# Performance work log

Measured on AMD Instinct MI355X. Metric: run time of the kernel, lower is better.

## Reference

```python
import jax, jax.numpy as jnp
import numpy as np

N_NODES = 50000
N_EDGES = 1600000
N_GRAPHS = 512
HEADS = 4
HEAD_DIM = 32
LAYERS = 3
NEG_SLOPE = 0.2


def setup_inputs() -> dict:
    key = jax.random.key(0)
    ks = jax.random.split(key, 7)
    x = jax.random.normal(ks[0], (N_NODES, 128), dtype=jnp.float32)
    Ws = jax.random.normal(ks[1], (LAYERS, 128, 128), dtype=jnp.float32) * 0.1
    att_src = jax.random.normal(ks[2], (LAYERS, HEADS, HEAD_DIM), dtype=jnp.float32) * 0.1
    att_dst = jax.random.normal(ks[3], (LAYERS, HEADS, HEAD_DIM), dtype=jnp.float32) * 0.1
    biases = jnp.zeros((LAYERS, 128), dtype=jnp.float32)
    edge_index = jax.random.randint(ks[4], (2, N_EDGES), 0, N_NODES, dtype=jnp.int64)
    batch = jnp.sort(jax.random.randint(ks[5], (N_NODES,), 0, N_GRAPHS, dtype=jnp.int64))
    return {"x": x, "Ws": Ws, "att_src": att_src, "att_dst": att_dst,
            "biases": biases, "edge_index": edge_index, "batch": batch}


def _gat_layer(x, W, a_s, a_d, b, src, dst, n):
    # linear transform -> per-head features [N, H, C]
    h = (x @ W).reshape(n, HEADS, HEAD_DIM)
    # per-node attention halves [N, H]
    alpha_src = jnp.einsum('nhc,hc->nh', h, a_s)
    alpha_dst = jnp.einsum('nhc,hc->nh', h, a_d)
    # edge logits [E, H]
    e = jax.nn.leaky_relu(alpha_src[src] + alpha_dst[dst], NEG_SLOPE)
    # segment softmax over incoming edges of each destination node
    m = jax.ops.segment_max(e, dst, num_segments=n)
    w = jnp.exp(e - m[dst])
    denom = jax.ops.segment_sum(w, dst, num_segments=n)
    alpha = w / (denom[dst] + 1e-16)
    # weighted scatter-add of source features [E, H, C] -> [N, H, C]
    msg = h[src] * alpha[:, :, None]
    out = jax.ops.segment_sum(msg, dst, num_segments=n)
    return out.reshape(n, HEADS * HEAD_DIM) + b


def reference(x, Ws, att_src, att_dst, biases, edge_index, batch):
    n = x.shape[0]
    # PyG GATConv adds self-loops by default
    loops = jnp.arange(n, dtype=edge_index.dtype)
    src = jnp.concatenate([edge_index[0], loops])
    dst = jnp.concatenate([edge_index[1], loops])
    for l in range(LAYERS):
        x = jax.nn.elu(_gat_layer(x, Ws[l], att_src[l], att_dst[l], biases[l], src, dst, n))
        # dropout is identity in eval mode
    # global mean pool over graphs
    sums = jax.ops.segment_sum(x, batch, num_segments=N_GRAPHS)
    cnt = jax.ops.segment_sum(jnp.ones((n,), x.dtype), batch, num_segments=N_GRAPHS)
    return sums / jnp.maximum(cnt, 1.0)[:, None]
```

## Files before the change

### kernel.cpp

```cpp
#include <hip/hip_runtime.h>
#include <hip/hip_fp16.h>
#include <math.h>

#define HEADS 4
#define HDIM 32
#define FD 128
#define NEG 0.2f
#define BCAP 4608
#define CH 8192
#define CHW 128

typedef _Float16 f16x8 __attribute__((ext_vector_type(8)));
typedef float f32x4 __attribute__((ext_vector_type(4)));

__device__ __forceinline__ float lrelu(float x) { return fmaxf(x, NEG * x); }

__global__ __launch_bounds__(256) void k_prepW(const float* __restrict__ W,
                                               _Float16* __restrict__ W16T) {
    int l = blockIdx.x;
    const float* Wl = W + (long)l * FD * FD;
    _Float16* o = W16T + (long)l * FD * FD;
    for (int i = threadIdx.x; i < FD * FD; i += 256) {
        int k = i >> 7, n = i & 127;
        o[n * FD + k] = (_Float16)Wl[i];
    }
}

__global__ __launch_bounds__(256) void k_cvt(const float* __restrict__ x,
                                             __half* __restrict__ o, long n) {
    long i = ((long)blockIdx.x * 256 + threadIdx.x) * 4;
    if (i < n) {
        float4 v = *(const float4*)&x[i];
        *(__half2*)&o[i] = __floats2half2_rn(v.x, v.y);
        *(__half2*)&o[i + 2] = __floats2half2_rn(v.z, v.w);
    }
}

__global__ __launch_bounds__(256) void k_gemm_mfma(const __half* __restrict__ x16,
                                                   const _Float16* __restrict__ W16T,
                                                   __half* __restrict__ h, int N) {
    __shared__ _Float16 wl[FD * FD];
    int t = threadIdx.x;
    for (int i = t * 8; i < FD * FD; i += 2048)
        *(f16x8*)&wl[i] = *(const f16x8*)&W16T[i];

    int w = t >> 6, lane = t & 63;
    int m = lane & 15, quad = lane >> 4;
    int row0 = blockIdx.x * 128 + w * 32;

    f16x8 a[2][4];
    f16x8 zf = {};
#pragma unroll
    for (int rt = 0; rt < 2; ++rt) {
        int gr = row0 + rt * 16 + m;
#pragma unroll
        for (int kc = 0; kc < 4; ++kc)
            a[rt][kc] = (gr < N) ? *(const f16x8*)&x16[(long)gr * FD + kc * 32 + quad * 8] : zf;
    }
    f32x4 acc[2][8];
#pragma unroll
    for (int rt = 0; rt < 2; ++rt)
#pragma unroll
        for (int c = 0; c < 8; ++c) acc[rt][c] = (f32x4){0.f, 0.f, 0.f, 0.f};

    __syncthreads();
#pragma unroll
    for (int c = 0; c < 8; ++c) {
        int nb = c * 16 + m;
#pragma unroll
        for (int kc = 0; kc < 4; ++kc) {
            f16x8 b = *(f16x8*)&wl[nb * FD + kc * 32 + quad * 8];
            acc[0][c] = __builtin_amdgcn_mfma_f32_16x16x32_f16(a[0][kc], b, acc[0][c], 0, 0, 0);
            acc[1][c] = __builtin_amdgcn_mfma_f32_16x16x32_f16(a[1][kc], b, acc[1][c], 0, 0, 0);
        }
    }
#pragma unroll
    for (int rt = 0; rt < 2; ++rt) {
        int rbase = row0 + rt * 16 + quad * 4;
#pragma unroll
        for (int c = 0; c < 8; ++c) {
            int col = c * 16 + m;
#pragma unroll
            for (int i = 0; i < 4; ++i) {
                int gr = rbase + i;
                if (gr < N) h[(long)gr * FD + col] = __float2half(acc[rt][c][i]);
            }
        }
    }
}

__global__ __launch_bounds__(256) void k_alpha(const __half* __restrict__ h,
                                               const float* __restrict__ a_s,
                                               const float* __restrict__ a_d,
                                               float* __restrict__ as_o,
                                               float* __restrict__ ad_o, int N) {
    int t = threadIdx.x;
    int n = blockIdx.x * 16 + (t >> 4);
    if (n >= N) return;
    int c16 = t & 15, gh = c16 >> 2, cb = c16 * 8;
    int c32 = (c16 & 3) * 8;
    float4 raw = *(const float4*)&h[(long)n * FD + cb];
    const __half* hh = (const __half*)&raw;
    float vs = 0.f, vd = 0.f;
#pragma unroll
    for (int i = 0; i < 8; ++i) {
        float hv = __half2float(hh[i]);
        vs += hv * a_s[gh * HDIM + c32 + i];
        vd += hv * a_d[gh * HDIM + c32 + i];
    }
    vs += __shfl_xor(vs, 1); vs += __shfl_xor(vs, 2);
    vd += __shfl_xor(vd, 1); vd += __shfl_xor(vd, 2);
    if ((c16 & 3) == 0) {
        as_o[n * HEADS + gh] = vs;
        ad_o[n * HEADS + gh] = vd;
    }
}

__global__ void k_zero_f(float* __restrict__ p, long n) {
    long i = (long)blockIdx.x * 256 + threadIdx.x;
    if (i < n) p[i] = 0.f;
}
__global__ void k_zero_i(int* __restrict__ p, int n) {
    int i = blockIdx.x * 256 + threadIdx.x;
    if (i < n) p[i] = 0;
}

__global__ __launch_bounds__(1024) void k_bin(const int* __restrict__ ei, int NE,
                                              int nbuck,
                                              int* __restrict__ bcnt,
                                              int* __restrict__ binned) {
    __shared__ int hist[512];
    __shared__ int gbase[512];
    int t = threadIdx.x;
    int c0 = blockIdx.x * CH;
    if (t < 512) hist[t] = 0;
    __syncthreads();
    int sub[8], val[8], loff[8];
#pragma unroll
    for (int k = 0; k < 8; ++k) {
        int idx = c0 + k * 1024 + t;
        sub[k] = -1;
        if (idx < NE) {
            int s = ei[idx], d = ei[NE + idx];
            sub[k] = d >> 7;
            val[k] = s | ((d & 127) << 16);
            loff[k] = atomicAdd(&hist[sub[k]], 1);
        }
    }
    __syncthreads();
    if (t < 512 && t < nbuck && hist[t] > 0)
        gbase[t] = atomicAdd(&bcnt[t], hist[t]);
    __syncthreads();
#pragma unroll
    for (int k = 0; k < 8; ++k) {
        if (sub[k] >= 0) {
            int p = gbase[sub[k]] + loff[k];
            if (p < BCAP) binned[(long)sub[k] * BCAP + p] = val[k];
        }
    }
}

__global__ __launch_bounds__(1024) void k_scan_sub(const int* __restrict__ bcnt,
                                                   int* __restrict__ bbase, int n,
                                                   int* __restrict__ rowstart, int N, int NE) {
    __shared__ int sm[1024];
    int t = threadIdx.x;
    int c0 = t * 4;
    int v0 = (c0 < n) ? bcnt[c0] : 0;
    int v1 = (c0 + 1 < n) ? bcnt[c0 + 1] : 0;
    int v2 = (c0 + 2 < n) ? bcnt[c0 + 2] : 0;
    int v3 = (c0 + 3 < n) ? bcnt[c0 + 3] : 0;
    int tot = v0 + v1 + v2 + v3;
    sm[t] = tot;
    __syncthreads();
    for (int off = 1; off < 1024; off <<= 1) {
        int u = (t >= off) ? sm[t - off] : 0;
        __syncthreads();
        sm[t] += u;
        __syncthreads();
    }
    int base = sm[t] - tot;
    if (c0 < n) bbase[c0] = base;
    if (c0 + 1 < n) bbase[c0 + 1] = base + v0;
    if (c0 + 2 < n) bbase[c0 + 2] = base + v0 + v1;
    if (c0 + 3 < n) bbase[c0 + 3] = base + v0 + v1 + v2;
    if (t == 1023) {
        bbase[n] = sm[1023];
        rowstart[N] = NE;
    }
}

__global__ __launch_bounds__(256) void k_bucket_csr(const int* __restrict__ binned,
                                                    const int* __restrict__ bcnt,
                                                    const int* __restrict__ bbase,
                                                    int* __restrict__ csr_src,
                                                    int* __restrict__ rowstart, int N) {
    int b = blockIdx.x;
    int t = threadIdx.x;
    __shared__ int ldeg[128], lofs[128], lcur[128];
    __shared__ int lcsr[BCAP];
    if (t < 128) ldeg[t] = 0;
    __syncthreads();
    int cnt = bcnt[b];
    if (cnt > BCAP) cnt = BCAP;
    int base = bbase[b];
    const int* reg = binned + (long)b * BCAP;
    for (int i = t; i < cnt; i += 256)
        atomicAdd(&ldeg[reg[i] >> 16], 1);
    __syncthreads();
    if (t < 128) lofs[t] = ldeg[t];
    __syncthreads();
    for (int off = 1; off < 128; off <<= 1) {
        int u = (t < 128 && t >= off) ? lofs[t - off] : 0;
        __syncthreads();
        if (t < 128) lofs[t] += u;
        __syncthreads();
    }
    if (t < 128) lcur[t] = lofs[t] - ldeg[t];
    __syncthreads();
    for (int i = t; i < cnt; i += 256) {
        int v = reg[i];
        int p = atomicAdd(&lcur[v >> 16], 1);
        lcsr[p] = v & 0xFFFF;
    }
    __syncthreads();
    for (int i = t; i < cnt; i += 256) csr_src[base + i] = lcsr[i];
    if (t < 128) {
        int d = b * 128 + t;
        if (d < N) rowstart[d] = base + lofs[t] - ldeg[t];
    }
}

__global__ __launch_bounds__(256) void k_aggr(const int* __restrict__ csr_src,
                                              const int* __restrict__ rowstart,
                                              const float* __restrict__ as_,
                                              const float* __restrict__ ad_,
                                              const __half* __restrict__ h,
                                              const float* __restrict__ bias,
                                              __half* __restrict__ out, int N) {
    __shared__ int s_all[4][CHW];
    int t = threadIdx.x;
    int wv = t >> 6, lane = t & 63;
    int n = blockIdx.x * 4 + wv;
    if (n >= N) return;
    int* s_lds = s_all[wv];
    int c16 = lane & 15, rg = lane >> 4;
    int gh = c16 >> 2;
    int cb = c16 * 8;
    int beg = rowstart[n], end = rowstart[n + 1];
    int deg = end - beg;
    float adn = ad_[n * HEADS + gh];
    float l = 0.f;
    float acc[8] = {0.f, 0.f, 0.f, 0.f, 0.f, 0.f, 0.f, 0.f};

    for (int c0 = 0; c0 < deg; c0 += CHW) {
        int cnt = deg - c0;
        if (cnt > CHW) cnt = CHW;
        for (int i = lane; i < cnt; i += 64) s_lds[i] = csr_src[beg + c0 + i];
        __builtin_amdgcn_wave_barrier();
        for (int e = rg; e < cnt; e += 4) {
            int s = s_lds[e];
            float lg = lrelu(as_[s * HEADS + gh] + adn);
            float w = __expf(fminf(lg, 30.f));
            l += w;
            float4 raw = *(const float4*)&h[(long)s * FD + cb];
            const __half* hh = (const __half*)&raw;
#pragma unroll
            for (int i = 0; i < 8; ++i)
                acc[i] += __half2float(hh[i]) * w;
        }
        __builtin_amdgcn_wave_barrier();
    }
    l += __shfl_xor(l, 16);
    l += __shfl_xor(l, 32);
#pragma unroll
    for (int i = 0; i < 8; ++i) {
        acc[i] += __shfl_xor(acc[i], 16);
        acc[i] += __shfl_xor(acc[i], 32);
    }
    if (rg == 0) {
        float sl = lrelu(as_[n * HEADS + gh] + adn);
        float sw = __expf(fminf(sl, 30.f));
        float inv = 1.f / (l + sw + 1e-16f);
        float4 rawh = *(const float4*)&h[(long)n * FD + cb];
        const __half* hh = (const __half*)&rawh;
        float4 b0 = *(const float4*)&bias[cb];
        float4 b1 = *(const float4*)&bias[cb + 4];
        float bb[8] = {b0.x, b0.y, b0.z, b0.w, b1.x, b1.y, b1.z, b1.w};
        __half o8[8];
#pragma unroll
        for (int i = 0; i < 8; ++i) {
            float v = (acc[i] + sw * __half2float(hh[i])) * inv + bb[i];
            o8[i] = __float2half(v > 0.f ? v : expm1f(v));
        }
        *(float4*)&out[(long)n * FD + cb] = *(float4*)o8;
    }
}

__global__ __launch_bounds__(128) void k_pool(const __half* __restrict__ x,
                                              const int* __restrict__ batch,
                                              float* __restrict__ out,
                                              float* __restrict__ cnt, int N) {
    int n0 = blockIdx.x * 128;
    if (n0 >= N) return;
    int n1 = n0 + 128;
    if (n1 > N) n1 = N;
    int ch = threadIdx.x;
    __shared__ int gb[128];
    if (n0 + ch < N) gb[ch] = batch[n0 + ch];
    __syncthreads();
    int g = gb[0];
    float sum = 0.f, c_local = 0.f;
    for (int n = n0; n < n1; ++n) {
        int gn = gb[n - n0];
        if (gn != g) {
            atomicAdd(&out[(long)g * FD + ch], sum);
            if (ch == 0) atomicAdd(&cnt[g], c_local);
            sum = 0.f;
            c_local = 0.f;
            g = gn;
        }
        sum += __half2float(x[(long)n * FD + ch]);
        c_local += 1.f;
    }
    atomicAdd(&out[(long)g * FD + ch], sum);
    if (ch == 0) atomicAdd(&cnt[g], c_local);
}

__global__ void k_div(float* __restrict__ out, const float* __restrict__ cnt, int G) {
    int i = blockIdx.x * 256 + threadIdx.x;
    if (i >= G * FD) return;
    float c = cnt[i >> 7];
    out[i] /= (c > 1.f ? c : 1.f);
}

extern "C" void kernel_launch(void* const* d_in, const int* in_sizes, int n_in,
                              void* d_out, int out_size, void* d_ws, size_t ws_size,
                              hipStream_t stream) {
    const float* x0     = (const float*)d_in[0];
    const float* Wall   = (const float*)d_in[1];
    const float* att_s  = (const float*)d_in[2];
    const float* att_d  = (const float*)d_in[3];
    const float* biases = (const float*)d_in[4];
    const int*   ei     = (const int*)d_in[5];
    const int*   batch  = (const int*)d_in[6];
    float*       out    = (float*)d_out;

    int N  = in_sizes[0] / FD;
    int NE = in_sizes[5] / 2;
    int G  = out_size / FD;

    int nbuck = (N + 127) >> 7;

    long nF = (long)N * FD;
    float*    wsf      = (float*)d_ws;
    float*    as_      = wsf;
    float*    ad_      = as_ + (long)N * HEADS;
    float*    cnt      = ad_ + (long)N * HEADS;
    int*      rowstart = (int*)(cnt + G);
    int*      bcnt     = rowstart + N + 1;
    int*      bbase    = bcnt + nbuck;
    int*      csr_src  = bbase + nbuck + 1;
    __half*   h        = (__half*)(csr_src + NE);
    __half*   x16      = h + nF;
    _Float16* W16T     = (_Float16*)(x16 + nF);
    int*      binned   = (int*)(W16T + 3 * FD * FD);

    k_zero_i<<<(nbuck + 255) / 256, 256, 0, stream>>>(bcnt, nbuck);
    k_bin<<<(NE + CH - 1) / CH, 1024, 0, stream>>>(ei, NE, nbuck, bcnt, binned);
    k_scan_sub<<<1, 1024, 0, stream>>>(bcnt, bbase, nbuck, rowstart, N, NE);
    k_bucket_csr<<<nbuck, 256, 0, stream>>>(binned, bcnt, bbase, csr_src, rowstart, N);
    k_prepW<<<3, 256, 0, stream>>>(Wall, W16T);
    k_cvt<<<(int)((nF / 4 + 255) / 256), 256, 0, stream>>>(x0, x16, nF);

    for (int l = 0; l < 3; ++l) {
        k_gemm_mfma<<<(N + 127) / 128, 256, 0, stream>>>(x16, W16T + (long)l * FD * FD, h, N);
        k_alpha<<<(N + 15) / 16, 256, 0, stream>>>(h, att_s + l * HEADS * HDIM,
                                                   att_d + l * HEADS * HDIM, as_, ad_, N);
        k_aggr<<<(N + 3) / 4, 256, 0, stream>>>(csr_src, rowstart, as_, ad_, h,
                                                biases + l * FD, x16, N);
    }

    k_zero_f<<<(G * FD + 255) / 256, 256, 0, stream>>>(out, G * FD);
    k_zero_f<<<(G + 255) / 256, 256, 0, stream>>>(cnt, G);
    k_pool<<<(N + 127) / 128, 128, 0, stream>>>(x16, batch, out, cnt, N);
    k_div<<<(G * FD + 255) / 256, 256, 0, stream>>>(out, cnt, G);
}
```

Before: 407.2 us.

## Fold next-layer attention logits into aggregation via precomputed W·att vectors

Precomputes W_l·att_src and W_l·att_dst per layer so the next layer's per-node attention halves can be computed in the aggregation epilogue. This removes two of the three k_alpha launches and their reread of h. The change also zeroes the count buffer inside the scan kernel, shrinks pooling blocks to 32 nodes for more parallelism, and unrolls the edge loop. The cost is extra epilogue work in every lane of k_aggr, double-buffered alpha arrays, and slightly different rounding, because the logits now come from fp32 activations rather than the fp16 GEMM output.

```diff
diff --git a/kernel.cpp b/kernel.cpp
--- a/kernel.cpp
+++ b/kernel.cpp
@@ -16,13 +16,30 @@
 __device__ __forceinline__ float lrelu(float x) { return fmaxf(x, NEG * x); }
 
 __global__ __launch_bounds__(256) void k_prepW(const float* __restrict__ W,
-                                               _Float16* __restrict__ W16T) {
+                                               const float* __restrict__ att_s,
+                                               const float* __restrict__ att_d,
+                                               _Float16* __restrict__ W16T,
+                                               float* __restrict__ va_s,
+                                               float* __restrict__ va_d) {
     int l = blockIdx.x;
     const float* Wl = W + (long)l * FD * FD;
     _Float16* o = W16T + (long)l * FD * FD;
     for (int i = threadIdx.x; i < FD * FD; i += 256) {
         int k = i >> 7, n = i & 127;
         o[n * FD + k] = (_Float16)Wl[i];
+    }
+    const float* as_l = att_s + l * HEADS * HDIM;
+    const float* ad_l = att_d + l * HEADS * HDIM;
+    for (int idx = threadIdx.x; idx < HEADS * FD; idx += 256) {
+        int hd = idx >> 7, k = idx & 127;
+        float ss = 0.f, dd = 0.f;
+        for (int c = 0; c < HDIM; ++c) {
+            float w = Wl[k * FD + hd * HDIM + c];
+            ss += w * as_l[hd * HDIM + c];
+            dd += w * ad_l[hd * HDIM + c];
+        }
+        va_s[(long)l * HEADS * FD + idx] = ss;
+        va_d[(long)l * HEADS * FD + idx] = dd;
     }
 }
 
@@ -162,9 +179,14 @@
 
 __global__ __launch_bounds__(1024) void k_scan_sub(const int* __restrict__ bcnt,
                                                    int* __restrict__ bbase, int n,
-                                                   int* __restrict__ rowstart, int N, int NE) {
+                                                   int* __restrict__ rowstart, int N, int NE,
+                                                   float* __restrict__ cnt, int G) {
     __shared__ int sm[1024];
     int t = threadIdx.x;
+    if (t >= 512) {
+        int i = t - 512;
+        if (i < G) cnt[i] = 0.f;
+    }
     int c0 = t * 4;
     int v0 = (c0 < n) ? bcnt[c0] : 0;
     int v1 = (c0 + 1 < n) ? bcnt[c0 + 1] : 0;
@@ -237,6 +259,10 @@
                                               const float* __restrict__ ad_,
                                               const __half* __restrict__ h,
                                               const float* __restrict__ bias,
+                                              const float* __restrict__ va_s,
+                                              const float* __restrict__ va_d,
+                                              float* __restrict__ as_n,
+                                              float* __restrict__ ad_n,
                                               __half* __restrict__ out, int N) {
     __shared__ int s_all[4][CHW];
     int t = threadIdx.x;
@@ -258,6 +284,7 @@
         if (cnt > CHW) cnt = CHW;
         for (int i = lane; i < cnt; i += 64) s_lds[i] = csr_src[beg + c0 + i];
         __builtin_amdgcn_wave_barrier();
+#pragma unroll 2
         for (int e = rg; e < cnt; e += 4) {
             int s = s_lds[e];
             float lg = lrelu(as_[s * HEADS + gh] + adn);
@@ -278,22 +305,43 @@
         acc[i] += __shfl_xor(acc[i], 16);
         acc[i] += __shfl_xor(acc[i], 32);
     }
+    float sl = lrelu(as_[n * HEADS + gh] + adn);
+    float sw = __expf(fminf(sl, 30.f));
+    float inv = 1.f / (l + sw + 1e-16f);
+    float4 rawh = *(const float4*)&h[(long)n * FD + cb];
+    const __half* hh = (const __half*)&rawh;
+    float4 b0 = *(const float4*)&bias[cb];
+    float4 b1 = *(const float4*)&bias[cb + 4];
+    float bb[8] = {b0.x, b0.y, b0.z, b0.w, b1.x, b1.y, b1.z, b1.w};
+    float v[8];
+#pragma unroll
+    for (int i = 0; i < 8; ++i) {
+        float u = (acc[i] + sw * __half2float(hh[i])) * inv + bb[i];
+        v[i] = u > 0.f ? u : expm1f(u);
+    }
     if (rg == 0) {
-        float sl = lrelu(as_[n * HEADS + gh] + adn);
-        float sw = __expf(fminf(sl, 30.f));
-        float inv = 1.f / (l + sw + 1e-16f);
-        float4 rawh = *(const float4*)&h[(long)n * FD + cb];
-        const __half* hh = (const __half*)&rawh;
-        float4 b0 = *(const float4*)&bias[cb];
-        float4 b1 = *(const float4*)&bias[cb + 4];
-        float bb[8] = {b0.x, b0.y, b0.z, b0.w, b1.x, b1.y, b1.z, b1.w};
         __half o8[8];
 #pragma unroll
+        for (int i = 0; i < 8; ++i) o8[i] = __float2half(v[i]);
+        *(float4*)&out[(long)n * FD + cb] = *(float4*)o8;
+    }
+    if (va_s) {
+        const float* vs = va_s + rg * FD + cb;
+        const float* vd = va_d + rg * FD + cb;
+        float ps = 0.f, pd = 0.f;
+#pragma unroll
         for (int i = 0; i < 8; ++i) {
-            float v = (acc[i] + sw * __half2float(hh[i])) * inv + bb[i];
-            o8[i] = __float2half(v > 0.f ? v : expm1f(v));
-        }
-        *(float4*)&out[(long)n * FD + cb] = *(float4*)o8;
+            ps += v[i] * vs[i];
+            pd += v[i] * vd[i];
+        }
+        for (int off = 1; off < 16; off <<= 1) {
+            ps += __shfl_xor(ps, off);
+            pd += __shfl_xor(pd, off);
+        }
+        if (c16 == 0) {
+            as_n[n * HEADS + rg] = ps;
+            ad_n[n * HEADS + rg] = pd;
+        }
     }
 }
 
@@ -301,13 +349,13 @@
                                               const int* __restrict__ batch,
                                               float* __restrict__ out,
                                               float* __restrict__ cnt, int N) {
-    int n0 = blockIdx.x * 128;
+    int n0 = blockIdx.x * 32;
     if (n0 >= N) return;
-    int n1 = n0 + 128;
+    int n1 = n0 + 32;
     if (n1 > N) n1 = N;
     int ch = threadIdx.x;
-    __shared__ int gb[128];
-    if (n0 + ch < N) gb[ch] = batch[n0 + ch];
+    __shared__ int gb[32];
+    if (ch < n1 - n0) gb[ch] = batch[n0 + ch];
     __syncthreads();
     int g = gb[0];
     float sum = 0.f, c_local = 0.f;
@@ -354,10 +402,14 @@
 
     long nF = (long)N * FD;
     float*    wsf      = (float*)d_ws;
-    float*    as_      = wsf;
-    float*    ad_      = as_ + (long)N * HEADS;
-    float*    cnt      = ad_ + (long)N * HEADS;
-    int*      rowstart = (int*)(cnt + G);
+    float*    asA      = wsf;
+    float*    adA      = asA + (long)N * HEADS;
+    float*    asB      = adA + (long)N * HEADS;
+    float*    adB      = asB + (long)N * HEADS;
+    float*    cnt      = adB + (long)N * HEADS;
+    float*    va_s     = cnt + G;
+    float*    va_d     = va_s + 3 * HEADS * FD;
+    int*      rowstart = (int*)(va_d + 3 * HEADS * FD);
     int*      bcnt     = rowstart + N + 1;
     int*      bbase    = bcnt + nbuck;
     int*      csr_src  = bbase + nbuck + 1;
@@ -368,21 +420,26 @@
 
     k_zero_i<<<(nbuck + 255) / 256, 256, 0, stream>>>(bcnt, nbuck);
     k_bin<<<(NE + CH - 1) / CH, 1024, 0, stream>>>(ei, NE, nbuck, bcnt, binned);
-    k_scan_sub<<<1, 1024, 0, stream>>>(bcnt, bbase, nbuck, rowstart, N, NE);
+    k_scan_sub<<<1, 1024, 0, stream>>>(bcnt, bbase, nbuck, rowstart, N, NE, cnt, G);
     k_bucket_csr<<<nbuck, 256, 0, stream>>>(binned, bcnt, bbase, csr_src, rowstart, N);
-    k_prepW<<<3, 256, 0, stream>>>(Wall, W16T);
+    k_prepW<<<3, 256, 0, stream>>>(Wall, att_s, att_d, W16T, va_s, va_d);
     k_cvt<<<(int)((nF / 4 + 255) / 256), 256, 0, stream>>>(x0, x16, nF);
 
+    float* asR[3] = {asA, asB, asA};
+    float* adR[3] = {adA, adB, adA};
     for (int l = 0; l < 3; ++l) {
         k_gemm_mfma<<<(N + 127) / 128, 256, 0, stream>>>(x16, W16T + (long)l * FD * FD, h, N);
-        k_alpha<<<(N + 15) / 16, 256, 0, stream>>>(h, att_s + l * HEADS * HDIM,
-                                                   att_d + l * HEADS * HDIM, as_, ad_, N);
-        k_aggr<<<(N + 3) / 4, 256, 0, stream>>>(csr_src, rowstart, as_, ad_, h,
-                                                biases + l * FD, x16, N);
+        if (l == 0)
+            k_alpha<<<(N + 15) / 16, 256, 0, stream>>>(h, att_s, att_d, asA, adA, N);
+        const float* vs = (l < 2) ? va_s + (long)(l + 1) * HEADS * FD : nullptr;
+        const float* vd = (l < 2) ? va_d + (long)(l + 1) * HEADS * FD : nullptr;
+        k_aggr<<<(N + 3) / 4, 256, 0, stream>>>(csr_src, rowstart, asR[l], adR[l], h,
+                                                biases + l * FD, vs, vd,
+                                                asR[l + 1 < 3 ? l + 1 : 0],
+                                                adR[l + 1 < 3 ? l + 1 : 0], x16, N);
     }
 
     k_zero_f<<<(G * FD + 255) / 256, 256, 0, stream>>>(out, G * FD);
-    k_zero_f<<<(G + 255) / 256, 256, 0, stream>>>(cnt, G);
-    k_pool<<<(N + 127) / 128, 128, 0, stream>>>(x16, batch, out, cnt, N);
+    k_pool<<<(N + 31) / 32, 128, 0, stream>>>(x16, batch, out, cnt, N);
     k_div<<<(G * FD + 255) / 256, 256, 0, stream>>>(out, cnt, G);
 }
```

Result: faster. 362.1 us (-11.1%).
